# Optimization experiments

Measured on AMD Instinct MI355X. Metric: run time of the kernel, lower is better.

The kernel has to match this reference:

```python
import jax, jax.numpy as jnp
import numpy as np

B_BASE = 512   # queries
F_IN = 16      # incoming beam width
F_OUT = 16     # outgoing beam width (cfg.B)
D = 128        # vector dim
DH = 256       # MLP hidden dim
KCB = 4096     # codebook size
A = 32         # n_codes: approximate top-k shortlist
M = 2          # previous code steps
L = 2          # residual blocks


def setup_inputs() -> dict:
    key = jax.random.key(0)
    ks = jax.random.split(key, 16)
    s = 0.05
    return {
        "x_BD": jax.random.normal(ks[0], (B_BASE, D), jnp.float32),
        "xhat_BFD": jax.random.normal(ks[1], (B_BASE, F_IN, D), jnp.float32),
        "codes_MBF": jax.random.randint(ks[2], (M, B_BASE, F_IN), 0, KCB),
        "codebook": jax.random.normal(ks[3], (KCB, D), jnp.float32) * s,
        "codebook_rq": jax.random.normal(ks[4], (KCB, D), jnp.float32) * s,
        "in_w": jax.random.normal(ks[5], (D, DH), jnp.float32) * s,
        "in_b": jnp.zeros((DH,), jnp.float32),
        "cc_w": jax.random.normal(ks[6], (DH + D, DH), jnp.float32) * s,
        "cc_b": jnp.zeros((DH,), jnp.float32),
        "rb_w1": jax.random.normal(ks[7], (L, DH, DH), jnp.float32) * s,
        "rb_b1": jnp.zeros((L, DH), jnp.float32),
        "rb_w2": jax.random.normal(ks[8], (L, DH, DH), jnp.float32) * s,
        "rb_b2": jnp.zeros((L, DH), jnp.float32),
        "out_w": jax.random.normal(ks[9], (DH, D), jnp.float32) * s,
        "out_b": jnp.zeros((D,), jnp.float32),
    }


def reference(x_BD, xhat_BFD, codes_MBF, codebook, codebook_rq,
              in_w, in_b, cc_w, cc_b, rb_w1, rb_b1, rb_w2, rb_b2,
              out_w, out_b):
    B_base, F, Dd = xhat_BFD.shape
    B = B_base * F
    xhat_BD = xhat_BFD.reshape(B, Dd)

    # --- stage 1: approximate pairwise distance (drops ||x||^2 term) + shortlist topk ---
    xt_BD = (x_BD[:, None, :] - xhat_BFD).reshape(B, Dd)           # residual targets
    cb_sq = jnp.sum(codebook_rq * codebook_rq, axis=-1)             # [K]
    dists_BK = cb_sq[None, :] - 2.0 * (xt_BD @ codebook_rq.T)       # [B, K]
    _, top_codes_BA = jax.lax.top_k(-dists_BK, A)                   # smallest-A -> [B, A]

    # --- stage 2: gather codewords, run small residual MLP on candidates ---
    cw_in = codebook[top_codes_BA].reshape(B_base, F, A, Dd)        # [Bb,F,A,D]
    h = cw_in @ in_w + in_b                                         # in_proj -> [Bb,F,A,DH]
    xb = jnp.broadcast_to(xhat_BFD[:, :, None, :], (B_base, F, A, Dd))
    h = jnp.concatenate([h, xb], axis=-1) @ cc_w + cc_b             # concat block
    for i in range(rb_w1.shape[0]):
        h = h + jax.nn.relu(h @ rb_w1[i] + rb_b1[i]) @ rb_w2[i] + rb_b2[i]
    cw = h @ out_w + out_b + cw_in                                   # out_proj + residual codeword

    # --- stage 3: exact-ish distance over beam*A candidates + beam topk ---
    cw = cw.reshape(B, A, Dd) + xhat_BD[:, None, :]                  # candidate reconstructions
    cw_flat = cw.reshape(B_base, F * A, Dd)
    d2 = jnp.sum(cw_flat * cw_flat, axis=-1) - 2.0 * jnp.einsum('bd,bkd->bk', x_BD, cw_flat)
    _, idx_BF = jax.lax.top_k(-d2, F_OUT)                            # [Bb, F_OUT]

    # --- stage 4: regather codes and reconstructions for surviving beams ---
    codes_g_BF = jnp.take_along_axis(top_codes_BA.reshape(B_base, F * A), idx_BF, axis=-1)
    codes_rep = jnp.repeat(codes_MBF, A, axis=-1)                    # [M,Bb,F*A]
    idx_M = jnp.broadcast_to(idx_BF[None], (codes_MBF.shape[0], B_base, F_OUT))
    codes_sel = jnp.take_along_axis(codes_rep, idx_M, axis=-1)       # [M,Bb,F_OUT]
    xhat_next = jnp.take_along_axis(cw_flat, idx_BF[:, :, None], axis=1)  # [Bb,F_OUT,D]
    codes_out = jnp.concatenate([codes_sel, codes_g_BF[None]], axis=0)    # [M+1,Bb,F_OUT]
    return xhat_next, codes_out
```

## Files before the change

### kernel.cpp

```cpp
#include <hip/hip_runtime.h>
#include <float.h>

typedef unsigned int u32;
typedef unsigned long long u64;
typedef unsigned short u16;
typedef __attribute__((ext_vector_type(8))) short s16x8;
typedef __attribute__((ext_vector_type(4))) float f32x4;


static __device__ __forceinline__ u32 ordu(float f) {
  u32 u = __float_as_uint(f);
  return u ^ (u32)(((int)u >> 31) | (int)0x80000000);
}
static __device__ __forceinline__ u16 f2bf(float f) {
  u32 b = __float_as_uint(f);
  b += 0x7fffu + ((b >> 16) & 1u);
  return (u16)(b >> 16);
}


__global__ __launch_bounds__(256) void k_cbrqT(const float* __restrict__ cbrq,
                                               float* __restrict__ cbT,
                                               float* __restrict__ cb_sq) {
  __shared__ float tile[128 * 33];
  const int k0 = blockIdx.x * 32;
  const int t = threadIdx.x;
#pragma unroll
  for (int rep = 0; rep < 16; ++rep) {
    const int flat = rep * 256 + t;
    const int kk = flat >> 7, d = flat & 127;
    tile[d * 33 + kk] = cbrq[(k0 + kk) * 128 + d];
  }
  __syncthreads();
#pragma unroll
  for (int rep = 0; rep < 16; ++rep) {
    const int flat = rep * 256 + t;
    const int d = flat >> 5, kk = flat & 31;
    cbT[d * 4096 + k0 + kk] = tile[d * 33 + kk];
  }
  if (t < 32) {
    float r[8];
#pragma unroll
    for (int j = 0; j < 8; ++j) {
      const float v = tile[j * 33 + t];
      r[j] = __fmul_rn(v, v);
    }
    for (int i = 8; i < 128; i += 8) {
#pragma unroll
      for (int j = 0; j < 8; ++j) {
        const float v = tile[(i + j) * 33 + t];
        r[j] = __fadd_rn(r[j], __fmul_rn(v, v));
      }
    }
    cb_sq[k0 + t] = __fadd_rn(
        __fadd_rn(__fadd_rn(r[0], r[1]), __fadd_rn(r[2], r[3])),
        __fadd_rn(__fadd_rn(r[4], r[5]), __fadd_rn(r[6], r[7])));
  }
}

__global__ __launch_bounds__(256) void k_codeh(const float* __restrict__ cb,
                                               const float* __restrict__ in_w,
                                               const float* __restrict__ in_b,
                                               const float* __restrict__ cc_w,
                                               float* __restrict__ tmp_h,
                                               float* __restrict__ P) {
  __shared__ float row[128];
  __shared__ float th[256];
  const int code = blockIdx.x;
  const int t = threadIdx.x;
  if (t < 128) row[t] = cb[code * 128 + t];
  __syncthreads();
  float a = 0.f;
  for (int d = 0; d < 128; ++d) a = __builtin_fmaf(row[d], in_w[d * 256 + t], a);
  const float thv = __fadd_rn(a, in_b[t]);
  tmp_h[code * 256 + t] = thv;
  th[t] = thv;
  __syncthreads();
  float p = 0.f;
  for (int i = 0; i < 256; i += 4) {
    const float w0 = cc_w[(i + 0) * 256 + t], w1 = cc_w[(i + 1) * 256 + t];
    const float w2 = cc_w[(i + 2) * 256 + t], w3 = cc_w[(i + 3) * 256 + t];
    p = __builtin_fmaf(th[i + 0], w0, p);
    p = __builtin_fmaf(th[i + 1], w1, p);
    p = __builtin_fmaf(th[i + 2], w2, p);
    p = __builtin_fmaf(th[i + 3], w3, p);
  }
  P[code * 256 + t] = p;
}

__global__ __launch_bounds__(256) void k_pack(const float* __restrict__ rb_w1,
                                              const float* __restrict__ out_w,
                                              float* __restrict__ Wcat) {
  const int i = blockIdx.x;
  const int t = threadIdx.x;
  Wcat[i * 640 + t] = rb_w1[i * 256 + t];
  Wcat[i * 640 + 256 + t] = rb_w1[65536 + i * 256 + t];
  if (t < 128) Wcat[i * 640 + 512 + t] = out_w[i * 128 + t];
}

__global__ __launch_bounds__(256) void k_biasprep(
    const float* __restrict__ rb_b1, const float* __restrict__ rb_b2,
    const float* __restrict__ rb_w1, const float* __restrict__ out_w,
    const float* __restrict__ out_b, const float* __restrict__ cc_b,
    const float* __restrict__ Wcat, float* __restrict__ cvec) {
  const int t = threadIdx.x;
  const float* w11 = rb_w1 + 65536;
  float b2v = rb_b1[256 + t];
  for (int i = 0; i < 256; ++i) b2v += rb_b2[i] * w11[i * 256 + t];
  float c0 = rb_b1[t], c1 = b2v;
  for (int i = 0; i < 256; ++i) {
    const float cbi = cc_b[i];
    c0 += cbi * Wcat[i * 640 + t];
    c1 += cbi * Wcat[i * 640 + 256 + t];
  }
  cvec[t] = c0;
  cvec[256 + t] = c1;
  if (t < 128) {
    float bDv = out_b[t];
    for (int i = 0; i < 256; ++i)
      bDv += (rb_b2[i] + rb_b2[256 + i]) * out_w[i * 128 + t];
    float c2 = bDv;
    for (int i = 0; i < 256; ++i) c2 += cc_b[i] * Wcat[i * 640 + 512 + t];
    cvec[512 + t] = c2;
  }
}

__global__ __launch_bounds__(256) void k_wfrag(
    const float* __restrict__ W21, const float* __restrict__ V1,
    const float* __restrict__ V2, u16* __restrict__ W21f,
    u16* __restrict__ V1f, u16* __restrict__ V2f) {
  const int gid = blockIdx.x * 256 + threadIdx.x;
  const int l = gid & 63;
  const int grp = gid >> 6;
  const int kq = (l >> 4) * 8;
  const int nn = l & 15;
  if (grp < 128) {
    const int kt = grp >> 4, nt = grp & 15;
    u16* dst = W21f + (size_t)(grp * 64 + l) * 8;
#pragma unroll
    for (int j = 0; j < 8; ++j)
      dst[j] = f2bf(W21[(kt * 32 + kq + j) * 256 + nt * 16 + nn]);
  } else if (grp < 192) {
    const int g2 = grp - 128, kt = g2 >> 3, nt = g2 & 7;
    u16* dst = V1f + (size_t)(g2 * 64 + l) * 8;
#pragma unroll
    for (int j = 0; j < 8; ++j)
      dst[j] = f2bf(V1[(kt * 32 + kq + j) * 128 + nt * 16 + nn]);
  } else {
    const int g2 = grp - 192, kt = g2 >> 3, nt = g2 & 7;
    u16* dst = V2f + (size_t)(g2 * 64 + l) * 8;
#pragma unroll
    for (int j = 0; j < 8; ++j)
      dst[j] = f2bf(V2[(kt * 32 + kq + j) * 128 + nt * 16 + nn]);
  }
}

__global__ __launch_bounds__(256, 4) void gemm_f32(
    const float* __restrict__ Am, const float* __restrict__ Bm,
    float* __restrict__ Cm, const int Mi, const int Ni, const int Ki,
    const float* __restrict__ bias, const float* __restrict__ addm) {
  __shared__ float As[16][68];
  __shared__ float Bs[16][68];
  const int m0 = blockIdx.x * 64, n0 = blockIdx.y * 64;
  const int t = threadIdx.x;
  const int tm = (t & 15) * 4, tn = (t >> 4) * 4;
  float acc[4][4] = {};
  for (int k0 = 0; k0 < Ki; k0 += 16) {
    {
      const int row = t >> 2, q = t & 3;
      const float4 a4 = *(const float4*)(Am + (size_t)(m0 + row) * Ki + k0 + q * 4);
      As[q * 4 + 0][row] = a4.x; As[q * 4 + 1][row] = a4.y;
      As[q * 4 + 2][row] = a4.z; As[q * 4 + 3][row] = a4.w;
      const int kk = t >> 4, n4 = t & 15;
      *(float4*)&Bs[kk][n4 * 4] =
          *(const float4*)(Bm + (size_t)(k0 + kk) * Ni + n0 + n4 * 4);
    }
    __syncthreads();
#pragma unroll
    for (int kk = 0; kk < 16; ++kk) {
      const float4 av = *(const float4*)&As[kk][tm];
      const float4 bv = *(const float4*)&Bs[kk][tn];
      const float aa[4] = {av.x, av.y, av.z, av.w};
      const float bb[4] = {bv.x, bv.y, bv.z, bv.w};
#pragma unroll
      for (int i = 0; i < 4; ++i)
#pragma unroll
        for (int j = 0; j < 4; ++j) acc[i][j] += aa[i] * bb[j];
    }
    __syncthreads();
  }
#pragma unroll
  for (int i = 0; i < 4; ++i) {
    const int m = m0 + tm + i;
#pragma unroll
    for (int j = 0; j < 4; ++j) {
      const int n = n0 + tn + j;
      float v = acc[i][j];
      if (bias) v += bias[n];
      if (addm) v += addm[(size_t)m * Ni + n];
      Cm[(size_t)m * Ni + n] = v;
    }
  }
}

__global__ __launch_bounds__(256, 4) void gemm_scatter(
    const float* __restrict__ Am, const float* __restrict__ Bm, const int Mi,
    const int Ki, const float* __restrict__ bias,
    const float* __restrict__ add3, float* __restrict__ O1,
    float* __restrict__ O2, float* __restrict__ O3) {
  __shared__ float As[16][68];
  __shared__ float Bs[16][68];
  const int m0 = blockIdx.x * 64, n0 = blockIdx.y * 64;
  const int t = threadIdx.x;
  const int tm = (t & 15) * 4, tn = (t >> 4) * 4;
  float acc[4][4] = {};
  for (int k0 = 0; k0 < Ki; k0 += 16) {
    {
      const int row = t >> 2, q = t & 3;
      const float4 a4 = *(const float4*)(Am + (size_t)(m0 + row) * Ki + k0 + q * 4);
      As[q * 4 + 0][row] = a4.x; As[q * 4 + 1][row] = a4.y;
      As[q * 4 + 2][row] = a4.z; As[q * 4 + 3][row] = a4.w;
      const int kk = t >> 4, n4 = t & 15;
      *(float4*)&Bs[kk][n4 * 4] =
          *(const float4*)(Bm + (size_t)(k0 + kk) * 640 + n0 + n4 * 4);
    }
    __syncthreads();
#pragma unroll
    for (int kk = 0; kk < 16; ++kk) {
      const float4 av = *(const float4*)&As[kk][tm];
      const float4 bv = *(const float4*)&Bs[kk][tn];
      const float aa[4] = {av.x, av.y, av.z, av.w};
      const float bb[4] = {bv.x, bv.y, bv.z, bv.w};
#pragma unroll
      for (int i = 0; i < 4; ++i)
#pragma unroll
        for (int j = 0; j < 4; ++j) acc[i][j] += aa[i] * bb[j];
    }
    __syncthreads();
  }
#pragma unroll
  for (int i = 0; i < 4; ++i) {
    const int m = m0 + tm + i;
#pragma unroll
    for (int j = 0; j < 4; ++j) {
      const int n = n0 + tn + j;
      float v = acc[i][j];
      if (bias) v += bias[n];
      if (n < 256) {
        O1[(size_t)m * 256 + n] = v;
      } else if (n < 512) {
        O2[(size_t)m * 256 + n - 256] = v;
      } else {
        if (add3) v += add3[(size_t)m * 128 + n - 512];
        O3[(size_t)m * 128 + n - 512] = v;
      }
    }
  }
}

__global__ __launch_bounds__(512, 2) void k_stage1(
    const float* __restrict__ x, const float* __restrict__ xhat,
    const float* __restrict__ cbT, const float* __restrict__ cb_sq,
    int* __restrict__ topc) {
  __shared__ u32 distL[4 * 4096];
  __shared__ float xtL[512];
  const int r0 = blockIdx.x * 4;
  const int t = threadIdx.x;
  {
    const int rr = r0 + (t >> 7), d = t & 127;
    xtL[t] = __fsub_rn(x[(rr >> 4) * 128 + d], xhat[rr * 128 + d]);
  }
  __syncthreads();
  {
    const int k0 = t * 8;
    float acc[4][8] = {};
    for (int d = 0; d < 128; ++d) {
      const float4 c0 = *(const float4*)&cbT[d * 4096 + k0];
      const float4 c1 = *(const float4*)&cbT[d * 4096 + k0 + 4];
      const float cv[8] = {c0.x, c0.y, c0.z, c0.w, c1.x, c1.y, c1.z, c1.w};
      const float x0 = xtL[d], x1 = xtL[128 + d], x2 = xtL[256 + d],
                  x3 = xtL[384 + d];
#pragma unroll
      for (int j = 0; j < 8; ++j) {
        acc[0][j] = __builtin_fmaf(x0, cv[j], acc[0][j]);
        acc[1][j] = __builtin_fmaf(x1, cv[j], acc[1][j]);
        acc[2][j] = __builtin_fmaf(x2, cv[j], acc[2][j]);
        acc[3][j] = __builtin_fmaf(x3, cv[j], acc[3][j]);
      }
    }
    const float4 s0 = *(const float4*)&cb_sq[k0];
    const float4 s1 = *(const float4*)&cb_sq[k0 + 4];
    const float cs[8] = {s0.x, s0.y, s0.z, s0.w, s1.x, s1.y, s1.z, s1.w};
#pragma unroll
    for (int rr = 0; rr < 4; ++rr)
#pragma unroll
      for (int j = 0; j < 8; ++j)
        distL[rr * 4096 + k0 + j] =
            ordu(__fsub_rn(cs[j], __fmul_rn(2.0f, acc[rr][j])));
  }
  __syncthreads();
  const int w = t >> 6, lane = t & 63;
  if (w < 4) {
    u32* dr = distL + w * 4096;
    u64 m1 = ~0ull, m2 = ~0ull;
    for (int e = 0; e < 64; ++e) {
      const int idx = e * 64 + lane;
      const u64 key = ((u64)dr[idx] << 32) | (u32)idx;
      if (key < m1) { m2 = m1; m1 = key; } else if (key < m2) { m2 = key; }
    }
    bool have2 = true;
    for (int it = 0; it < 32; ++it) {
      u64 g = m1;
#pragma unroll
      for (int sh = 1; sh < 64; sh <<= 1) {
        const u64 o = __shfl_xor(g, sh);
        g = (o < g) ? o : g;
      }
      const int bi = (int)(g & 0xFFFFFFFFu);
      if (lane == 0) topc[(r0 + w) * 32 + it] = bi;
      if ((bi & 63) == lane) {
        dr[bi] = 0xFFFFFFFFu;
        if (have2) {
          m1 = m2; m2 = ~0ull; have2 = false;
        } else {
          m1 = m2 = ~0ull;
          for (int e = 0; e < 64; ++e) {
            const int idx = e * 64 + lane;
            const u64 key = ((u64)dr[idx] << 32) | (u32)idx;
            if (key < m1) { m2 = m1; m1 = key; } else if (key < m2) { m2 = key; }
          }
          have2 = true;
        }
      }
    }
  }
}

__global__ __launch_bounds__(256, 4) void k_mlp(
    const int* __restrict__ topc, const float* __restrict__ A1,
    const float* __restrict__ A2, const float* __restrict__ B1,
    const float* __restrict__ B2, const float* __restrict__ Dc,
    const float* __restrict__ Dr, const u16* __restrict__ W21f,
    const u16* __restrict__ V1f, const u16* __restrict__ V2f,
    const float* __restrict__ xhat, const float* __restrict__ x,
    float* __restrict__ d2g) {
  __shared__ __align__(16) u16 abuf[32 * 264];
  __shared__ float B1r[256];
  __shared__ int codesL[32];
  __shared__ float d2red[32][4];

  const int tt = threadIdx.x;
  const int br = blockIdx.x;
  const int bb = br >> 4;
  const int w = tt >> 6, l = tt & 63;

  B1r[tt] = B1[br * 256 + tt];
  if (tt < 32) codesL[tt] = topc[br * 32 + tt];
  __syncthreads();

  {
    const int c = tt & 31, g = tt >> 5;
    const int code = codesL[c];
    const float4* A14 = (const float4*)(A1 + code * 256 + g * 32);
    u32* dst = (u32*)(abuf + c * 264 + g * 32);
#pragma unroll
// ... 37 lines not shown

  f32x4 acc2f[2][2];
#pragma unroll
  for (int mt = 0; mt < 2; ++mt)
#pragma unroll
    for (int ntl = 0; ntl < 2; ++ntl) acc2f[mt][ntl] = zero4;
  for (int kt = 0; kt < 8; ++kt) {
    const s16x8 a0 = *(const s16x8*)(abuf + arow * 264 + kt * 32 + kq);
    const s16x8 a1 = *(const s16x8*)(abuf + (16 + arow) * 264 + kt * 32 + kq);
#pragma unroll
    for (int ntl = 0; ntl < 2; ++ntl) {
      const s16x8 b = v1f[(kt * 8 + w * 2 + ntl) * 64 + l];
      acc2f[0][ntl] = __builtin_amdgcn_mfma_f32_16x16x32_bf16(
          a0, b, acc2f[0][ntl], 0, 0, 0);
      acc2f[1][ntl] = __builtin_amdgcn_mfma_f32_16x16x32_bf16(
          a1, b, acc2f[1][ntl], 0, 0, 0);
    }
  }

  u16 r2v[2][4][4];
#pragma unroll
  for (int mt = 0; mt < 2; ++mt)
#pragma unroll
    for (int ntl = 0; ntl < 4; ++ntl) {
      const int n = w * 64 + ntl * 16 + arow;
      const float b2 = B2[br * 256 + n];
      const f32x4 cf = accf[mt][ntl];
#pragma unroll
      for (int rg = 0; rg < 4; ++rg) {
        const int m = mt * 16 + (l >> 4) * 4 + rg;
        const float a2 = A2[codesL[m] * 256 + n];
        r2v[mt][ntl][rg] = f2bf(fmaxf(cf[rg] + a2 + b2, 0.f));
      }
    }
  __syncthreads();
#pragma unroll
  for (int mt = 0; mt < 2; ++mt)
#pragma unroll
    for (int ntl = 0; ntl < 4; ++ntl) {
      const int n = w * 64 + ntl * 16 + arow;
#pragma unroll
      for (int rg = 0; rg < 4; ++rg) {
        const int m = mt * 16 + (l >> 4) * 4 + rg;
        abuf[m * 264 + n] = r2v[mt][ntl][rg];
      }
    }
  __syncthreads();

  for (int kt = 0; kt < 8; ++kt) {
    const s16x8 a0 = *(const s16x8*)(abuf + arow * 264 + kt * 32 + kq);
    const s16x8 a1 = *(const s16x8*)(abuf + (16 + arow) * 264 + kt * 32 + kq);
#pragma unroll
    for (int ntl = 0; ntl < 2; ++ntl) {
      const s16x8 b = v2f[(kt * 8 + w * 2 + ntl) * 64 + l];
      acc2f[0][ntl] = __builtin_amdgcn_mfma_f32_16x16x32_bf16(
          a0, b, acc2f[0][ntl], 0, 0, 0);
      acc2f[1][ntl] = __builtin_amdgcn_mfma_f32_16x16x32_bf16(
          a1, b, acc2f[1][ntl], 0, 0, 0);
    }
  }

  float sm[2][4];
#pragma unroll
  for (int mt = 0; mt < 2; ++mt)
#pragma unroll
    for (int rg = 0; rg < 4; ++rg) sm[mt][rg] = 0.f;
#pragma unroll
  for (int ntl = 0; ntl < 2; ++ntl) {
    const int d = w * 32 + ntl * 16 + arow;
    const float dr = Dr[br * 128 + d];
    const float xh = xhat[br * 128 + d];
    const float xq = x[bb * 128 + d];
#pragma unroll
    for (int mt = 0; mt < 2; ++mt) {
      const f32x4 cf = acc2f[mt][ntl];
#pragma unroll
      for (int rg = 0; rg < 4; ++rg) {
        const int m = mt * 16 + (l >> 4) * 4 + rg;
        const float cand = cf[rg] + Dc[codesL[m] * 128 + d] + dr + xh;
        sm[mt][rg] += cand * cand - 2.f * xq * cand;
      }
    }
  }
#pragma unroll
  for (int mt = 0; mt < 2; ++mt)
#pragma unroll
    for (int rg = 0; rg < 4; ++rg) {
      float s = sm[mt][rg];
      s += __shfl_xor(s, 1);
      s += __shfl_xor(s, 2);
      s += __shfl_xor(s, 4);
      s += __shfl_xor(s, 8);
      if (arow == 0) d2red[mt * 16 + (l >> 4) * 4 + rg][w] = s;
    }
  __syncthreads();
  if (tt < 32)
    d2g[bb * 512 + (br & 15) * 32 + tt] =
        d2red[tt][0] + d2red[tt][1] + d2red[tt][2] + d2red[tt][3];
}

__global__ __launch_bounds__(64, 1) void k_sel32(const float* __restrict__ d2g,
                                                 int* __restrict__ sel32) {
  __shared__ u32 d2u[512];
  const int bb = blockIdx.x;
  const int t = threadIdx.x;
  for (int i = t; i < 512; i += 64) d2u[i] = ordu(d2g[bb * 512 + i]);
  __syncthreads();
  for (int it = 0; it < 32; ++it) {
    u64 m = ~0ull;
#pragma unroll
    for (int e = 0; e < 8; ++e) {
      const int idx = e * 64 + t;
      const u64 key = ((u64)d2u[idx] << 32) | (u32)idx;
      m = (key < m) ? key : m;
    }
#pragma unroll
    for (int sh = 1; sh < 64; sh <<= 1) {
      const u64 o = __shfl_xor(m, sh);
      m = (o < m) ? o : m;
    }
    const int s = (int)(m & 0xFFFFFFFFu);
    if ((s & 63) == t) d2u[s] = 0xFFFFFFFFu;
    if (t == 0) sel32[bb * 32 + it] = s;
  }
}

__global__ __launch_bounds__(256, 5) void k_rescore(
    const int* __restrict__ sel32, const int* __restrict__ topc,
    const float* __restrict__ P, const float* __restrict__ cb,
    const float* __restrict__ xhat, const float* __restrict__ x,
    const float* __restrict__ cc_w, const float* __restrict__ cc_b,
    const float* __restrict__ rb_w1, const float* __restrict__ rb_b1,
    const float* __restrict__ rb_w2, const float* __restrict__ rb_b2,
    const float* __restrict__ out_w, const float* __restrict__ out_b,
    float* __restrict__ d2r, float* __restrict__ candv) {
  __shared__ float A_[8][256], B_[8][256], C_[8][256];
  __shared__ float xhL[8][128], xqL[128];
  __shared__ int codeL[8], rowL[8];
  const int bb = blockIdx.x >> 2;
  const int j0 = (blockIdx.x & 3) * 8;
  const int t = threadIdx.x;
  if (t < 8) {
    const int s = sel32[bb * 32 + j0 + t];
    rowL[t] = bb * 16 + (s >> 5);
    codeL[t] = topc[(bb * 16 + (s >> 5)) * 32 + (s & 31)];
  }
  if (t < 128) xqL[t] = x[bb * 128 + t];
  __syncthreads();
  for (int idx = t; idx < 1024; idx += 256) {
    const int c = idx >> 7, d = idx & 127;
    xhL[c][d] = xhat[rowL[c] * 128 + d];
  }
  __syncthreads();
  {
    float acc[8];
#pragma unroll
    for (int c = 0; c < 8; ++c) acc[c] = P[codeL[c] * 256 + t];
    for (int d = 0; d < 128; d += 4) {
      const float w0 = cc_w[(256 + d + 0) * 256 + t];
      const float w1 = cc_w[(256 + d + 1) * 256 + t];
      const float w2 = cc_w[(256 + d + 2) * 256 + t];
      const float w3 = cc_w[(256 + d + 3) * 256 + t];
#pragma unroll
      for (int c = 0; c < 8; ++c) {
        const float4 h = *(const float4*)&xhL[c][d];
        acc[c] = __builtin_fmaf(h.x, w0, acc[c]);
        acc[c] = __builtin_fmaf(h.y, w1, acc[c]);
        acc[c] = __builtin_fmaf(h.z, w2, acc[c]);
        acc[c] = __builtin_fmaf(h.w, w3, acc[c]);
      }
    }
    const float b = cc_b[t];
#pragma unroll
    for (int c = 0; c < 8; ++c) B_[c][t] = __fadd_rn(acc[c], b);
  }
  __syncthreads();
  {
    float acc[8] = {};
    for (int i = 0; i < 256; i += 4) {
      const float w0 = rb_w1[(i + 0) * 256 + t], w1 = rb_w1[(i + 1) * 256 + t];
      const float w2 = rb_w1[(i + 2) * 256 + t], w3 = rb_w1[(i + 3) * 256 + t];
#pragma unroll
      for (int c = 0; c < 8; ++c) {
        const float4 h = *(const float4*)&B_[c][i];
        acc[c] = __builtin_fmaf(h.x, w0, acc[c]);
        acc[c] = __builtin_fmaf(h.y, w1, acc[c]);
        acc[c] = __builtin_fmaf(h.z, w2, acc[c]);
        acc[c] = __builtin_fmaf(h.w, w3, acc[c]);
      }
    }
    const float b = rb_b1[t];
#pragma unroll
    for (int c = 0; c < 8; ++c) C_[c][t] = fmaxf(__fadd_rn(acc[c], b), 0.f);
  }
  __syncthreads();
  {
    float acc[8] = {};
    for (int i = 0; i < 256; i += 4) {
      const float w0 = rb_w2[(i + 0) * 256 + t], w1 = rb_w2[(i + 1) * 256 + t];
      const float w2 = rb_w2[(i + 2) * 256 + t], w3 = rb_w2[(i + 3) * 256 + t];
#pragma unroll
      for (int c = 0; c < 8; ++c) {
        const float4 h = *(const float4*)&C_[c][i];
        acc[c] = __builtin_fmaf(h.x, w0, acc[c]);
        acc[c] = __builtin_fmaf(h.y, w1, acc[c]);
        acc[c] = __builtin_fmaf(h.z, w2, acc[c]);
        acc[c] = __builtin_fmaf(h.w, w3, acc[c]);
      }
    }
    const float b = rb_b2[t];
#pragma unroll
    for (int c = 0; c < 8; ++c)
      A_[c][t] = __fadd_rn(__fadd_rn(B_[c][t], acc[c]), b);
  }
  __syncthreads();
  {
    float acc[8] = {};
    const float* w11 = rb_w1 + 65536;
    for (int i = 0; i < 256; i += 4) {
      const float w0 = w11[(i + 0) * 256 + t], w1 = w11[(i + 1) * 256 + t];
      const float w2 = w11[(i + 2) * 256 + t], w3 = w11[(i + 3) * 256 + t];
#pragma unroll
      for (int c = 0; c < 8; ++c) {
        const float4 h = *(const float4*)&A_[c][i];
        acc[c] = __builtin_fmaf(h.x, w0, acc[c]);
        acc[c] = __builtin_fmaf(h.y, w1, acc[c]);
        acc[c] = __builtin_fmaf(h.z, w2, acc[c]);
        acc[c] = __builtin_fmaf(h.w, w3, acc[c]);
      }
    }
    const float b = rb_b1[256 + t];
#pragma unroll
    for (int c = 0; c < 8; ++c) B_[c][t] = fmaxf(__fadd_rn(acc[c], b), 0.f);
  }
  __syncthreads();
  {
    float acc[8] = {};
    const float* w21 = rb_w2 + 65536;
    for (int i = 0; i < 256; i += 4) {
      const float w0 = w21[(i + 0) * 256 + t], w1 = w21[(i + 1) * 256 + t];
      const float w2 = w21[(i + 2) * 256 + t], w3 = w21[(i + 3) * 256 + t];
#pragma unroll
      for (int c = 0; c < 8; ++c) {
        const float4 h = *(const float4*)&B_[c][i];
        acc[c] = __builtin_fmaf(h.x, w0, acc[c]);
        acc[c] = __builtin_fmaf(h.y, w1, acc[c]);
        acc[c] = __builtin_fmaf(h.z, w2, acc[c]);
        acc[c] = __builtin_fmaf(h.w, w3, acc[c]);
      }
    }
    const float b = rb_b2[256 + t];
#pragma unroll
    for (int c = 0; c < 8; ++c)
      C_[c][t] = __fadd_rn(__fadd_rn(A_[c][t], acc[c]), b);
  }
  __syncthreads();
  if (t < 128) {
    float acc[8] = {};
    for (int i = 0; i < 256; i += 4) {
      const float w0 = out_w[(i + 0) * 128 + t], w1 = out_w[(i + 1) * 128 + t];
      const float w2 = out_w[(i + 2) * 128 + t], w3 = out_w[(i + 3) * 128 + t];
#pragma unroll
      for (int c = 0; c < 8; ++c) {
        const float4 h = *(const float4*)&C_[c][i];
        acc[c] = __builtin_fmaf(h.x, w0, acc[c]);
        acc[c] = __builtin_fmaf(h.y, w1, acc[c]);
        acc[c] = __builtin_fmaf(h.z, w2, acc[c]);
        acc[c] = __builtin_fmaf(h.w, w3, acc[c]);
      }
    }
    const float ob = out_b[t];
#pragma unroll
    for (int c = 0; c < 8; ++c) {
      const float cbv = cb[codeL[c] * 128 + t];
      const float cw_ = __fadd_rn(__fadd_rn(acc[c], ob), cbv);
      const float cand = __fadd_rn(cw_, xhL[c][t]);
      B_[c][t] = cand;
      candv[(bb * 32 + j0 + c) * 128 + t] = cand;
    }
  }
  __syncthreads();
  if (t < 8) {
    float r[8];
#pragma unroll
    for (int j = 0; j < 8; ++j) {
      const float v = B_[t][j];
      r[j] = __fmul_rn(v, v);
    }
    for (int i = 8; i < 128; i += 8) {
#pragma unroll
      for (int j = 0; j < 8; ++j) {
        const float v = B_[t][i + j];
        r[j] = __fadd_rn(r[j], __fmul_rn(v, v));
      }
    }
    const float s1f = __fadd_rn(
        __fadd_rn(__fadd_rn(r[0], r[1]), __fadd_rn(r[2], r[3])),
        __fadd_rn(__fadd_rn(r[4], r[5]), __fadd_rn(r[6], r[7])));
    double s2 = 0.0;
    for (int d = 0; d < 128; ++d)
      s2 += (double)xqL[d] * (double)B_[t][d];
    const float s2f = (float)s2;
    d2r[bb * 32 + j0 + t] = __fsub_rn(s1f, __fmul_rn(2.0f, s2f));
  }
}

__global__ __launch_bounds__(64, 1) void k_final(
    const float* __restrict__ d2r, const int* __restrict__ sel32,
    const int* __restrict__ topc, const int* __restrict__ codes_in,
    const float* __restrict__ candv, float* __restrict__ out) {
  __shared__ u32 winLo[16];
  const int bb = blockIdx.x;
  const int t = threadIdx.x;
  u64 key = ~0ull;
  if (t < 32) {
    const u32 s = (u32)sel32[bb * 32 + t];
    key = ((u64)ordu(d2r[bb * 32 + t]) << 32) | (s << 5) | (u32)t;
  }
  for (int it = 0; it < 16; ++it) {
    u64 m = key;
#pragma unroll
    for (int sh = 1; sh < 64; sh <<= 1) {
      const u64 o = __shfl_xor(m, sh);
      m = (o < m) ? o : m;
    }
    if (key == m) key = ~0ull;
    if (t == 0) winLo[it] = (u32)(m & 0xFFFFFFFFu);
  }
  __syncthreads();
  if (t < 16) {
    const u32 lo = winLo[t];
    const int s = (int)((lo >> 5) & 511u);
    const int f = s >> 5;
    const int code = topc[(bb * 16 + f) * 32 + (s & 31)];
    float* oc = out + 512 * 16 * 128;
    oc[bb * 16 + t] = (float)codes_in[bb * 16 + f];
    oc[8192 + bb * 16 + t] = (float)codes_in[8192 + bb * 16 + f];
    oc[16384 + bb * 16 + t] = (float)code;
  }
  __syncthreads();
  for (int idx = t; idx < 2048; idx += 64) {
    const int w_ = idx >> 7, d = idx & 127;
    const int j = (int)(winLo[w_] & 31u);
    out[(bb * 16 + w_) * 128 + d] = candv[(bb * 32 + j) * 128 + d];
  }
}

extern "C" void kernel_launch(void* const* d_in, const int* in_sizes, int n_in,
                              void* d_out, int out_size, void* d_ws,
                              size_t ws_size, hipStream_t stream) {
  const float* x = (const float*)d_in[0];
  const float* xhat = (const float*)d_in[1];
  const int* codes = (const int*)d_in[2];
  const float* cb = (const float*)d_in[3];
  const float* cbrq = (const float*)d_in[4];
  const float* in_w = (const float*)d_in[5];
  const float* in_b = (const float*)d_in[6];
  const float* cc_w = (const float*)d_in[7];
  const float* cc_b = (const float*)d_in[8];
  const float* rb_w1 = (const float*)d_in[9];
  const float* rb_b1 = (const float*)d_in[10];
  const float* rb_w2 = (const float*)d_in[11];
  const float* rb_b2 = (const float*)d_in[12];
  const float* out_w = (const float*)d_in[13];
  const float* out_b = (const float*)d_in[14];
  float* out = (float*)d_out;

  float* ws = (float*)d_ws;
  size_t o = 0;
  float* cb_sq = ws + o; o += 4096;
  float* P = ws + o;     o += (size_t)4096 * 256;
  float* cbT = ws + o;   const size_t cbT_off = o; o += (size_t)128 * 4096;
  float* tmp_h = ws + o; o += (size_t)4096 * 256;
  float* Wcat = ws + o;  o += (size_t)256 * 640;
  float* M_A = ws + o;   o += (size_t)256 * 640;
  float* M_B = ws + o;   o += (size_t)128 * 640;
  float* cvec = ws + o;  o += 640;
  float* A1 = ws + o;    o += (size_t)4096 * 256;
  float* A2 = ws + o;    o += (size_t)4096 * 256;
  float* Dc = ws + o;    o += (size_t)4096 * 128;
  float* B1 = ws + o;    o += (size_t)8192 * 256;
  float* B2 = ws + o;    o += (size_t)8192 * 256;
  float* Dr = ws + o;    o += (size_t)8192 * 128;
  float* W21 = ws + o;   o += 65536;
  float* V1 = ws + o;    o += 32768;
  float* V2 = ws + o;    o += 32768;
  int* topc = (int*)(ws + o); o += 262144;
  float* d2g = ws + o;   o += 262144;
  u16* W21f = (u16*)(ws + o); o += 32768;
  u16* V1f = (u16*)(ws + o);  o += 16384;
  u16* V2f = (u16*)(ws + o);  o += 16384;
  float* candv = ws + o; o += (size_t)16384 * 128;
  float* d2r = ws + cbT_off;
  int* sel32 = (int*)(ws + cbT_off + 16384);

  k_cbrqT<<<dim3(128), dim3(256), 0, stream>>>(cbrq, cbT, cb_sq);
  k_codeh<<<dim3(4096), dim3(256), 0, stream>>>(cb, in_w, in_b, cc_w, tmp_h, P);
  k_pack<<<dim3(256), dim3(256), 0, stream>>>(rb_w1, out_w, Wcat);
  k_biasprep<<<dim3(1), dim3(256), 0, stream>>>(rb_b1, rb_b2, rb_w1, out_w,
                                                out_b, cc_b, Wcat, cvec);
  gemm_f32<<<dim3(4, 10), dim3(256), 0, stream>>>(cc_w, Wcat, M_A, 256, 640,
                                                  256, nullptr, nullptr);
  gemm_f32<<<dim3(2, 10), dim3(256), 0, stream>>>(cc_w + 256 * 256, Wcat, M_B,
                                                  128, 640, 256, nullptr,
                                                  nullptr);
  gemm_scatter<<<dim3(64, 10), dim3(256), 0, stream>>>(
      tmp_h, M_A, 4096, 256, nullptr, cb, A1, A2, Dc);
  gemm_scatter<<<dim3(128, 10), dim3(256), 0, stream>>>(
      xhat, M_B, 8192, 128, cvec, nullptr, B1, B2, Dr);
  gemm_f32<<<dim3(4, 4), dim3(256), 0, stream>>>(rb_w2, rb_w1 + 65536, W21, 256,
                                                 256, 256, nullptr, nullptr);
  gemm_f32<<<dim3(4, 2), dim3(256), 0, stream>>>(rb_w2, out_w, V1, 256, 128,
                                                 256, nullptr, nullptr);
  gemm_f32<<<dim3(4, 2), dim3(256), 0, stream>>>(rb_w2 + 65536, out_w, V2, 256,
                                                 128, 256, nullptr, nullptr);
  k_wfrag<<<dim3(64), dim3(256), 0, stream>>>(W21, V1, V2, W21f, V1f, V2f);

  k_stage1<<<dim3(2048), dim3(512), 0, stream>>>(x, xhat, cbT, cb_sq, topc);
  k_mlp<<<dim3(8192), dim3(256), 0, stream>>>(topc, A1, A2, B1, B2, Dc, Dr,
                                              W21f, V1f, V2f, xhat, x, d2g);
  k_sel32<<<dim3(512), dim3(64), 0, stream>>>(d2g, sel32);
  k_rescore<<<dim3(2048), dim3(256), 0, stream>>>(
      sel32, topc, P, cb, xhat, x, cc_w, cc_b, rb_w1, rb_b1, rb_w2, rb_b2,
      out_w, out_b, d2r, candv);
  k_final<<<dim3(512), dim3(64), 0, stream>>>(d2r, sel32, topc, codes, candv,
                                              out);
  (void)in_sizes; (void)n_in; (void)out_size; (void)ws_size;
}
```

Baseline: 878.4 us.

## Merge prep kernels into one launch and restructure rescore MLP thread mapping

Folds the codebook transpose, code hidden projection, bias prep, weight packing and the W21/V1/V2 weight-product-plus-bf16-fragment kernels into a single multi-role k_prep1 launch. The bias prep now reads rb_w1 and out_w directly instead of depending on Wcat, which the fused kernel writes in parallel. The two scatter GEMMs are merged into one launch. The rescore MLP is remapped so each thread computes two output columns for four candidates instead of one column for eight, which changes register use and weight reuse. The aim is to cut launch count and serialization among small prep kernels, at the risk of slow naive per-thread fp32 weight products in the fused prep blocks.

```diff
diff --git a/kernel.cpp b/kernel.cpp
--- a/kernel.cpp
+++ b/kernel.cpp
@@ -18,140 +18,177 @@
   return (u16)(b >> 16);
 }
 
-
-__global__ __launch_bounds__(256) void k_cbrqT(const float* __restrict__ cbrq,
-                                               float* __restrict__ cbT,
-                                               float* __restrict__ cb_sq) {
-  __shared__ float tile[128 * 33];
-  const int k0 = blockIdx.x * 32;
+static __device__ __forceinline__ void layer_fma(
+    const float* __restrict__ src, int srcStride, int c0, int jc,
+    const float* __restrict__ wbase, int klen, float a0[4], float a1[4]) {
+  for (int i = 0; i < klen; i += 4) {
+    const float wa0 = wbase[(i + 0) * 256 + jc];
+    const float wa1 = wbase[(i + 1) * 256 + jc];
+    const float wa2 = wbase[(i + 2) * 256 + jc];
+    const float wa3 = wbase[(i + 3) * 256 + jc];
+    const float wb0 = wbase[(i + 0) * 256 + jc + 128];
+    const float wb1 = wbase[(i + 1) * 256 + jc + 128];
+    const float wb2 = wbase[(i + 2) * 256 + jc + 128];
+    const float wb3 = wbase[(i + 3) * 256 + jc + 128];
+#pragma unroll
+    for (int c4 = 0; c4 < 4; ++c4) {
+      const float4 h = *(const float4*)&src[(c0 + c4) * srcStride + i];
+      a0[c4] = __builtin_fmaf(h.x, wa0, a0[c4]);
+      a0[c4] = __builtin_fmaf(h.y, wa1, a0[c4]);
+      a0[c4] = __builtin_fmaf(h.z, wa2, a0[c4]);
+      a0[c4] = __builtin_fmaf(h.w, wa3, a0[c4]);
+      a1[c4] = __builtin_fmaf(h.x, wb0, a1[c4]);
+      a1[c4] = __builtin_fmaf(h.y, wb1, a1[c4]);
+      a1[c4] = __builtin_fmaf(h.z, wb2, a1[c4]);
+      a1[c4] = __builtin_fmaf(h.w, wb3, a1[c4]);
+    }
+  }
+}
+
+__global__ __launch_bounds__(256) void k_prep1(
+    const float* __restrict__ cbrq, float* __restrict__ cbT,
+    float* __restrict__ cb_sq, const float* __restrict__ cb,
+    const float* __restrict__ in_w, const float* __restrict__ in_b,
+    const float* __restrict__ cc_w, float* __restrict__ tmp_h,
+    float* __restrict__ P, const float* __restrict__ rb_b1,
+    const float* __restrict__ rb_b2, const float* __restrict__ rb_w1,
+    const float* __restrict__ out_w, const float* __restrict__ out_b,
+    const float* __restrict__ cc_b, float* __restrict__ cvec,
+    float* __restrict__ Wcat, const float* __restrict__ rb_w2,
+    u16* __restrict__ W21f, u16* __restrict__ V1f, u16* __restrict__ V2f) {
+  __shared__ float sh[128 * 33];
+  const int b = blockIdx.x;
   const int t = threadIdx.x;
-#pragma unroll
-  for (int rep = 0; rep < 16; ++rep) {
-    const int flat = rep * 256 + t;
-    const int kk = flat >> 7, d = flat & 127;
-    tile[d * 33 + kk] = cbrq[(k0 + kk) * 128 + d];
-  }
-  __syncthreads();
-#pragma unroll
-  for (int rep = 0; rep < 16; ++rep) {
-    const int flat = rep * 256 + t;
-    const int d = flat >> 5, kk = flat & 31;
-    cbT[d * 4096 + k0 + kk] = tile[d * 33 + kk];
-  }
-  if (t < 32) {
-    float r[8];
-#pragma unroll
-    for (int j = 0; j < 8; ++j) {
-      const float v = tile[j * 33 + t];
-      r[j] = __fmul_rn(v, v);
-    }
-    for (int i = 8; i < 128; i += 8) {
+  if (b < 128) {
+    const int k0 = b * 32;
+#pragma unroll
+    for (int rep = 0; rep < 16; ++rep) {
+      const int flat = rep * 256 + t;
+      const int kk = flat >> 7, d = flat & 127;
+      sh[d * 33 + kk] = cbrq[(k0 + kk) * 128 + d];
+    }
+    __syncthreads();
+#pragma unroll
+    for (int rep = 0; rep < 16; ++rep) {
+      const int flat = rep * 256 + t;
+      const int d = flat >> 5, kk = flat & 31;
+      cbT[d * 4096 + k0 + kk] = sh[d * 33 + kk];
+    }
+    if (t < 32) {
+      float r[8];
 #pragma unroll
       for (int j = 0; j < 8; ++j) {
-        const float v = tile[(i + j) * 33 + t];
-        r[j] = __fadd_rn(r[j], __fmul_rn(v, v));
-      }
-    }
-    cb_sq[k0 + t] = __fadd_rn(
-        __fadd_rn(__fadd_rn(r[0], r[1]), __fadd_rn(r[2], r[3])),
-        __fadd_rn(__fadd_rn(r[4], r[5]), __fadd_rn(r[6], r[7])));
-  }
-}
-
-__global__ __launch_bounds__(256) void k_codeh(const float* __restrict__ cb,
-                                               const float* __restrict__ in_w,
-                                               const float* __restrict__ in_b,
-                                               const float* __restrict__ cc_w,
-                                               float* __restrict__ tmp_h,
-                                               float* __restrict__ P) {
-  __shared__ float row[128];
-  __shared__ float th[256];
-  const int code = blockIdx.x;
-  const int t = threadIdx.x;
-  if (t < 128) row[t] = cb[code * 128 + t];
-  __syncthreads();
-  float a = 0.f;
-  for (int d = 0; d < 128; ++d) a = __builtin_fmaf(row[d], in_w[d * 256 + t], a);
-  const float thv = __fadd_rn(a, in_b[t]);
-  tmp_h[code * 256 + t] = thv;
-  th[t] = thv;
-  __syncthreads();
-  float p = 0.f;
-  for (int i = 0; i < 256; i += 4) {
-    const float w0 = cc_w[(i + 0) * 256 + t], w1 = cc_w[(i + 1) * 256 + t];
-    const float w2 = cc_w[(i + 2) * 256 + t], w3 = cc_w[(i + 3) * 256 + t];
-    p = __builtin_fmaf(th[i + 0], w0, p);
-    p = __builtin_fmaf(th[i + 1], w1, p);
-    p = __builtin_fmaf(th[i + 2], w2, p);
-    p = __builtin_fmaf(th[i + 3], w3, p);
-  }
-  P[code * 256 + t] = p;
-}
-
-__global__ __launch_bounds__(256) void k_pack(const float* __restrict__ rb_w1,
-                                              const float* __restrict__ out_w,
-                                              float* __restrict__ Wcat) {
-  const int i = blockIdx.x;
-  const int t = threadIdx.x;
-  Wcat[i * 640 + t] = rb_w1[i * 256 + t];
-  Wcat[i * 640 + 256 + t] = rb_w1[65536 + i * 256 + t];
-  if (t < 128) Wcat[i * 640 + 512 + t] = out_w[i * 128 + t];
-}
-
-__global__ __launch_bounds__(256) void k_biasprep(
-    const float* __restrict__ rb_b1, const float* __restrict__ rb_b2,
-    const float* __restrict__ rb_w1, const float* __restrict__ out_w,
-    const float* __restrict__ out_b, const float* __restrict__ cc_b,
-    const float* __restrict__ Wcat, float* __restrict__ cvec) {
-  const int t = threadIdx.x;
-  const float* w11 = rb_w1 + 65536;
-  float b2v = rb_b1[256 + t];
-  for (int i = 0; i < 256; ++i) b2v += rb_b2[i] * w11[i * 256 + t];
-  float c0 = rb_b1[t], c1 = b2v;
-  for (int i = 0; i < 256; ++i) {
-    const float cbi = cc_b[i];
-    c0 += cbi * Wcat[i * 640 + t];
-    c1 += cbi * Wcat[i * 640 + 256 + t];
-  }
-  cvec[t] = c0;
-  cvec[256 + t] = c1;
-  if (t < 128) {
-    float bDv = out_b[t];
-    for (int i = 0; i < 256; ++i)
-      bDv += (rb_b2[i] + rb_b2[256 + i]) * out_w[i * 128 + t];
-    float c2 = bDv;
-    for (int i = 0; i < 256; ++i) c2 += cc_b[i] * Wcat[i * 640 + 512 + t];
-    cvec[512 + t] = c2;
-  }
-}
-
-__global__ __launch_bounds__(256) void k_wfrag(
-    const float* __restrict__ W21, const float* __restrict__ V1,
-    const float* __restrict__ V2, u16* __restrict__ W21f,
-    u16* __restrict__ V1f, u16* __restrict__ V2f) {
-  const int gid = blockIdx.x * 256 + threadIdx.x;
-  const int l = gid & 63;
-  const int grp = gid >> 6;
-  const int kq = (l >> 4) * 8;
-  const int nn = l & 15;
-  if (grp < 128) {
-    const int kt = grp >> 4, nt = grp & 15;
-    u16* dst = W21f + (size_t)(grp * 64 + l) * 8;
-#pragma unroll
-    for (int j = 0; j < 8; ++j)
-      dst[j] = f2bf(W21[(kt * 32 + kq + j) * 256 + nt * 16 + nn]);
-  } else if (grp < 192) {
-    const int g2 = grp - 128, kt = g2 >> 3, nt = g2 & 7;
-    u16* dst = V1f + (size_t)(g2 * 64 + l) * 8;
-#pragma unroll
-    for (int j = 0; j < 8; ++j)
-      dst[j] = f2bf(V1[(kt * 32 + kq + j) * 128 + nt * 16 + nn]);
+        const float v = sh[j * 33 + t];
+        r[j] = __fmul_rn(v, v);
+      }
+      for (int i = 8; i < 128; i += 8) {
+#pragma unroll
+        for (int j = 0; j < 8; ++j) {
+          const float v = sh[(i + j) * 33 + t];
+          r[j] = __fadd_rn(r[j], __fmul_rn(v, v));
+        }
+      }
+      cb_sq[k0 + t] = __fadd_rn(
+          __fadd_rn(__fadd_rn(r[0], r[1]), __fadd_rn(r[2], r[3])),
+          __fadd_rn(__fadd_rn(r[4], r[5]), __fadd_rn(r[6], r[7])));
+    }
+  } else if (b < 4224) {
+    const int code = b - 128;
+    float* row = sh;
+    float* th = sh + 128;
+    if (t < 128) row[t] = cb[code * 128 + t];
+    __syncthreads();
+    float a = 0.f;
+    for (int d = 0; d < 128; ++d)
+      a = __builtin_fmaf(row[d], in_w[d * 256 + t], a);
+    const float thv = __fadd_rn(a, in_b[t]);
+    tmp_h[code * 256 + t] = thv;
+    th[t] = thv;
+    __syncthreads();
+    float p = 0.f;
+    for (int i = 0; i < 256; i += 4) {
+      const float w0 = cc_w[(i + 0) * 256 + t], w1 = cc_w[(i + 1) * 256 + t];
+      const float w2 = cc_w[(i + 2) * 256 + t], w3 = cc_w[(i + 3) * 256 + t];
+      p = __builtin_fmaf(th[i + 0], w0, p);
+      p = __builtin_fmaf(th[i + 1], w1, p);
+      p = __builtin_fmaf(th[i + 2], w2, p);
+      p = __builtin_fmaf(th[i + 3], w3, p);
+    }
+    P[code * 256 + t] = p;
+  } else if (b == 4224) {
+    const float* w11 = rb_w1 + 65536;
+    float b2v = rb_b1[256 + t];
+    for (int i = 0; i < 256; ++i) b2v += rb_b2[i] * w11[i * 256 + t];
+    float c0 = rb_b1[t], c1 = b2v;
+    for (int i = 0; i < 256; ++i) {
+      const float cbi = cc_b[i];
+      c0 += cbi * rb_w1[i * 256 + t];
+      c1 += cbi * w11[i * 256 + t];
+    }
+    cvec[t] = c0;
+    cvec[256 + t] = c1;
+    if (t < 128) {
+      float bDv = out_b[t];
+      for (int i = 0; i < 256; ++i)
+        bDv += (rb_b2[i] + rb_b2[256 + i]) * out_w[i * 128 + t];
+      float c2 = bDv;
+      for (int i = 0; i < 256; ++i) c2 += cc_b[i] * out_w[i * 128 + t];
+      cvec[512 + t] = c2;
+    }
+  } else if (b < 4481) {
+    const int i = b - 4225;
+    Wcat[i * 640 + t] = rb_w1[i * 256 + t];
+    Wcat[i * 640 + 256 + t] = rb_w1[65536 + i * 256 + t];
+    if (t < 128) Wcat[i * 640 + 512 + t] = out_w[i * 128 + t];
   } else {
-    const int g2 = grp - 192, kt = g2 >> 3, nt = g2 & 7;
-    u16* dst = V2f + (size_t)(g2 * 64 + l) * 8;
-#pragma unroll
-    for (int j = 0; j < 8; ++j)
-      dst[j] = f2bf(V2[(kt * 32 + kq + j) * 128 + nt * 16 + nn]);
+    const int gid = (b - 4481) * 256 + t;
+    const int l = gid & 63;
+    const int grp = gid >> 6;
+    const int kq = (l >> 4) * 8;
+    const int nn = l & 15;
+    float acc[8] = {};
+    if (grp < 128) {
+      const int kt = grp >> 4, nt = grp & 15;
+      const int col = nt * 16 + nn;
+      const int r0 = kt * 32 + kq;
+      const float* w11 = rb_w1 + 65536;
+      for (int k = 0; k < 256; ++k) {
+        const float wv = w11[k * 256 + col];
+#pragma unroll
+        for (int j = 0; j < 8; ++j)
+          acc[j] = __builtin_fmaf(rb_w2[(r0 + j) * 256 + k], wv, acc[j]);
+      }
+      u16* dst = W21f + (size_t)(grp * 64 + l) * 8;
+#pragma unroll
+      for (int j = 0; j < 8; ++j) dst[j] = f2bf(acc[j]);
+    } else if (grp < 192) {
+      const int g2 = grp - 128, kt = g2 >> 3, nt = g2 & 7;
+      const int col = nt * 16 + nn;
+      const int r0 = kt * 32 + kq;
+      for (int k = 0; k < 256; ++k) {
+        const float wv = out_w[k * 128 + col];
+#pragma unroll
+        for (int j = 0; j < 8; ++j)
+          acc[j] = __builtin_fmaf(rb_w2[(r0 + j) * 256 + k], wv, acc[j]);
+      }
+      u16* dst = V1f + (size_t)(g2 * 64 + l) * 8;
+#pragma unroll
+      for (int j = 0; j < 8; ++j) dst[j] = f2bf(acc[j]);
+    } else {
+      const int g2 = grp - 192, kt = g2 >> 3, nt = g2 & 7;
+      const int col = nt * 16 + nn;
+      const int r0 = kt * 32 + kq;
+      const float* w21 = rb_w2 + 65536;
+      for (int k = 0; k < 256; ++k) {
+        const float wv = out_w[k * 128 + col];
+#pragma unroll
+        for (int j = 0; j < 8; ++j)
+          acc[j] = __builtin_fmaf(w21[(r0 + j) * 256 + k], wv, acc[j]);
+      }
+      u16* dst = V2f + (size_t)(g2 * 64 + l) * 8;
+#pragma unroll
+      for (int j = 0; j < 8; ++j) dst[j] = f2bf(acc[j]);
+    }
   }
 }
 
@@ -203,14 +240,25 @@
   }
 }
 
-__global__ __launch_bounds__(256, 4) void gemm_scatter(
-    const float* __restrict__ Am, const float* __restrict__ Bm, const int Mi,
-    const int Ki, const float* __restrict__ bias,
-    const float* __restrict__ add3, float* __restrict__ O1,
-    float* __restrict__ O2, float* __restrict__ O3) {
+__global__ __launch_bounds__(256, 4) void gemm_scatter2(
+    const float* __restrict__ tmp_h, const float* __restrict__ M_A,
+    const float* __restrict__ xhat, const float* __restrict__ M_B,
+    const float* __restrict__ cvec, const float* __restrict__ cb,
+    float* __restrict__ A1, float* __restrict__ A2, float* __restrict__ Dc,
+    float* __restrict__ B1, float* __restrict__ B2, float* __restrict__ Dr) {
   __shared__ float As[16][68];
   __shared__ float Bs[16][68];
-  const int m0 = blockIdx.x * 64, n0 = blockIdx.y * 64;
+  const bool isA = blockIdx.x < 64;
+  const float* Am = isA ? tmp_h : xhat;
+  const float* Bm = isA ? M_A : M_B;
+  const int Ki = isA ? 256 : 128;
+  const float* bias = isA ? nullptr : cvec;
+  const float* add3 = isA ? cb : nullptr;
+  float* O1 = isA ? A1 : B1;
+  float* O2 = isA ? A2 : B2;
+  float* O3 = isA ? Dc : Dr;
+  const int m0 = (isA ? blockIdx.x : blockIdx.x - 64) * 64;
+  const int n0 = blockIdx.y * 64;
   const int t = threadIdx.x;
   const int tm = (t & 15) * 4, tn = (t >> 4) * 4;
   float acc[4][4] = {};
@@ -554,131 +602,100 @@
     xhL[c][d] = xhat[rowL[c] * 128 + d];
   }
   __syncthreads();
+  const int hc = t >> 7;
+  const int c0 = hc * 4;
+  const int jc = t & 127;
+  float a0[4], a1[4];
+
+#pragma unroll
+  for (int c4 = 0; c4 < 4; ++c4) {
+    a0[c4] = P[codeL[c0 + c4] * 256 + jc];
+    a1[c4] = P[codeL[c0 + c4] * 256 + jc + 128];
+  }
+  layer_fma(&xhL[0][0], 128, c0, jc, cc_w + 256 * 256, 128, a0, a1);
   {
-    float acc[8];
-#pragma unroll
-    for (int c = 0; c < 8; ++c) acc[c] = P[codeL[c] * 256 + t];
-    for (int d = 0; d < 128; d += 4) {
-      const float w0 = cc_w[(256 + d + 0) * 256 + t];
-      const float w1 = cc_w[(256 + d + 1) * 256 + t];
-      const float w2 = cc_w[(256 + d + 2) * 256 + t];
-      const float w3 = cc_w[(256 + d + 3) * 256 + t];
-#pragma unroll
-      for (int c = 0; c < 8; ++c) {
-        const float4 h = *(const float4*)&xhL[c][d];
-        acc[c] = __builtin_fmaf(h.x, w0, acc[c]);
-        acc[c] = __builtin_fmaf(h.y, w1, acc[c]);
-        acc[c] = __builtin_fmaf(h.z, w2, acc[c]);
-        acc[c] = __builtin_fmaf(h.w, w3, acc[c]);
-      }
-    }
-    const float b = cc_b[t];
-#pragma unroll
-    for (int c = 0; c < 8; ++c) B_[c][t] = __fadd_rn(acc[c], b);
-  }
-  __syncthreads();
+    const float ba = cc_b[jc], bbv = cc_b[jc + 128];
+#pragma unroll
+    for (int c4 = 0; c4 < 4; ++c4) {
+      B_[c0 + c4][jc] = __fadd_rn(a0[c4], ba);
+      B_[c0 + c4][jc + 128] = __fadd_rn(a1[c4], bbv);
+    }
+  }
+  __syncthreads();
+#pragma unroll
+  for (int c4 = 0; c4 < 4; ++c4) { a0[c4] = 0.f; a1[c4] = 0.f; }
+  layer_fma(&B_[0][0], 256, c0, jc, rb_w1, 256, a0, a1);
   {
-    float acc[8] = {};
+    const float ba = rb_b1[jc], bbv = rb_b1[jc + 128];
+#pragma unroll
+    for (int c4 = 0; c4 < 4; ++c4) {
+      C_[c0 + c4][jc] = fmaxf(__fadd_rn(a0[c4], ba), 0.f);
+      C_[c0 + c4][jc + 128] = fmaxf(__fadd_rn(a1[c4], bbv), 0.f);
+    }
+  }
+  __syncthreads();
+#pragma unroll
+  for (int c4 = 0; c4 < 4; ++c4) { a0[c4] = 0.f; a1[c4] = 0.f; }
+  layer_fma(&C_[0][0], 256, c0, jc, rb_w2, 256, a0, a1);
+  {
+    const float ba = rb_b2[jc], bbv = rb_b2[jc + 128];
+#pragma unroll
+    for (int c4 = 0; c4 < 4; ++c4) {
+      A_[c0 + c4][jc] = __fadd_rn(__fadd_rn(B_[c0 + c4][jc], a0[c4]), ba);
+      A_[c0 + c4][jc + 128] =
+          __fadd_rn(__fadd_rn(B_[c0 + c4][jc + 128], a1[c4]), bbv);
+    }
+  }
+  __syncthreads();
+#pragma unroll
+  for (int c4 = 0; c4 < 4; ++c4) { a0[c4] = 0.f; a1[c4] = 0.f; }
+  layer_fma(&A_[0][0], 256, c0, jc, rb_w1 + 65536, 256, a0, a1);
+  {
+    const float ba = rb_b1[256 + jc], bbv = rb_b1[256 + jc + 128];
+#pragma unroll
+    for (int c4 = 0; c4 < 4; ++c4) {
+      B_[c0 + c4][jc] = fmaxf(__fadd_rn(a0[c4], ba), 0.f);
+      B_[c0 + c4][jc + 128] = fmaxf(__fadd_rn(a1[c4], bbv), 0.f);
+    }
+  }
+  __syncthreads();
+#pragma unroll
+  for (int c4 = 0; c4 < 4; ++c4) { a0[c4] = 0.f; a1[c4] = 0.f; }
+  layer_fma(&B_[0][0], 256, c0, jc, rb_w2 + 65536, 256, a0, a1);
+  {
+    const float ba = rb_b2[256 + jc], bbv = rb_b2[256 + jc + 128];
+#pragma unroll
+    for (int c4 = 0; c4 < 4; ++c4) {
+      C_[c0 + c4][jc] = __fadd_rn(__fadd_rn(A_[c0 + c4][jc], a0[c4]), ba);
+      C_[c0 + c4][jc + 128] =
+          __fadd_rn(__fadd_rn(A_[c0 + c4][jc + 128], a1[c4]), bbv);
+    }
+  }
+  __syncthreads();
+  {
+    const int d = jc;
+    float acc[4] = {};
     for (int i = 0; i < 256; i += 4) {
-      const float w0 = rb_w1[(i + 0) * 256 + t], w1 = rb_w1[(i + 1) * 256 + t];
-      const float w2 = rb_w1[(i + 2) * 256 + t], w3 = rb_w1[(i + 3) * 256 + t];
-#pragma unroll
-      for (int c = 0; c < 8; ++c) {
-        const float4 h = *(const float4*)&B_[c][i];
-        acc[c] = __builtin_fmaf(h.x, w0, acc[c]);
-        acc[c] = __builtin_fmaf(h.y, w1, acc[c]);
-        acc[c] = __builtin_fmaf(h.z, w2, acc[c]);
-        acc[c] = __builtin_fmaf(h.w, w3, acc[c]);
-      }
-    }
-    const float b = rb_b1[t];
-#pragma unroll
-    for (int c = 0; c < 8; ++c) C_[c][t] = fmaxf(__fadd_rn(acc[c], b), 0.f);
-  }
-  __syncthreads();
-  {
-    float acc[8] = {};
-    for (int i = 0; i < 256; i += 4) {
-      const float w0 = rb_w2[(i + 0) * 256 + t], w1 = rb_w2[(i + 1) * 256 + t];
-      const float w2 = rb_w2[(i + 2) * 256 + t], w3 = rb_w2[(i + 3) * 256 + t];
-#pragma unroll
-      for (int c = 0; c < 8; ++c) {
-        const float4 h = *(const float4*)&C_[c][i];
-        acc[c] = __builtin_fmaf(h.x, w0, acc[c]);
-        acc[c] = __builtin_fmaf(h.y, w1, acc[c]);
-        acc[c] = __builtin_fmaf(h.z, w2, acc[c]);
-        acc[c] = __builtin_fmaf(h.w, w3, acc[c]);
-      }
-    }
-    const float b = rb_b2[t];
-#pragma unroll
-    for (int c = 0; c < 8; ++c)
-      A_[c][t] = __fadd_rn(__fadd_rn(B_[c][t], acc[c]), b);
-  }
-  __syncthreads();
-  {
-    float acc[8] = {};
-    const float* w11 = rb_w1 + 65536;
-    for (int i = 0; i < 256; i += 4) {
-      const float w0 = w11[(i + 0) * 256 + t], w1 = w11[(i + 1) * 256 + t];
-      const float w2 = w11[(i + 2) * 256 + t], w3 = w11[(i + 3) * 256 + t];
-#pragma unroll
-      for (int c = 0; c < 8; ++c) {
-        const float4 h = *(const float4*)&A_[c][i];
-        acc[c] = __builtin_fmaf(h.x, w0, acc[c]);
-        acc[c] = __builtin_fmaf(h.y, w1, acc[c]);
-        acc[c] = __builtin_fmaf(h.z, w2, acc[c]);
-        acc[c] = __builtin_fmaf(h.w, w3, acc[c]);
-      }
-    }
-    const float b = rb_b1[256 + t];
-#pragma unroll
-    for (int c = 0; c < 8; ++c) B_[c][t] = fmaxf(__fadd_rn(acc[c], b), 0.f);
-  }
-  __syncthreads();
-  {
-    float acc[8] = {};
-    const float* w21 = rb_w2 + 65536;
-    for (int i = 0; i < 256; i += 4) {
-      const float w0 = w21[(i + 0) * 256 + t], w1 = w21[(i + 1) * 256 + t];
-      const float w2 = w21[(i + 2) * 256 + t], w3 = w21[(i + 3) * 256 + t];
-#pragma unroll
-      for (int c = 0; c < 8; ++c) {
-        const float4 h = *(const float4*)&B_[c][i];
-        acc[c] = __builtin_fmaf(h.x, w0, acc[c]);
-        acc[c] = __builtin_fmaf(h.y, w1, acc[c]);
-        acc[c] = __builtin_fmaf(h.z, w2, acc[c]);
-        acc[c] = __builtin_fmaf(h.w, w3, acc[c]);
-      }
-    }
-    const float b = rb_b2[256 + t];
-#pragma unroll
-    for (int c = 0; c < 8; ++c)
-      C_[c][t] = __fadd_rn(__fadd_rn(A_[c][t], acc[c]), b);
-  }
-  __syncthreads();
-  if (t < 128) {
-    float acc[8] = {};
-    for (int i = 0; i < 256; i += 4) {
-      const float w0 = out_w[(i + 0) * 128 + t], w1 = out_w[(i + 1) * 128 + t];
-      const float w2 = out_w[(i + 2) * 128 + t], w3 = out_w[(i + 3) * 128 + t];
-#pragma unroll
-      for (int c = 0; c < 8; ++c) {
-        const float4 h = *(const float4*)&C_[c][i];
-        acc[c] = __builtin_fmaf(h.x, w0, acc[c]);
-        acc[c] = __builtin_fmaf(h.y, w1, acc[c]);
-        acc[c] = __builtin_fmaf(h.z, w2, acc[c]);
-        acc[c] = __builtin_fmaf(h.w, w3, acc[c]);
-      }
-    }
-    const float ob = out_b[t];
-#pragma unroll
-    for (int c = 0; c < 8; ++c) {
-      const float cbv = cb[codeL[c] * 128 + t];
-      const float cw_ = __fadd_rn(__fadd_rn(acc[c], ob), cbv);
-      const float cand = __fadd_rn(cw_, xhL[c][t]);
-      B_[c][t] = cand;
-      candv[(bb * 32 + j0 + c) * 128 + t] = cand;
+      const float w0 = out_w[(i + 0) * 128 + d], w1 = out_w[(i + 1) * 128 + d];
+      const float w2 = out_w[(i + 2) * 128 + d], w3 = out_w[(i + 3) * 128 + d];
+#pragma unroll
+      for (int c4 = 0; c4 < 4; ++c4) {
+        const float4 h = *(const float4*)&C_[c0 + c4][i];
+        acc[c4] = __builtin_fmaf(h.x, w0, acc[c4]);
+        acc[c4] = __builtin_fmaf(h.y, w1, acc[c4]);
+        acc[c4] = __builtin_fmaf(h.z, w2, acc[c4]);
+        acc[c4] = __builtin_fmaf(h.w, w3, acc[c4]);
+      }
+    }
+    const float ob = out_b[d];
+#pragma unroll
+    for (int c4 = 0; c4 < 4; ++c4) {
+      const int c = c0 + c4;
+      const float cbv = cb[codeL[c] * 128 + d];
+      const float cw_ = __fadd_rn(__fadd_rn(acc[c4], ob), cbv);
+      const float cand = __fadd_rn(cw_, xhL[c][d]);
+      B_[c][d] = cand;
+      candv[(bb * 32 + j0 + c) * 128 + d] = cand;
     }
   }
   __syncthreads();
@@ -784,9 +801,6 @@
   float* B1 = ws + o;    o += (size_t)8192 * 256;
   float* B2 = ws + o;    o += (size_t)8192 * 256;
   float* Dr = ws + o;    o += (size_t)8192 * 128;
-  float* W21 = ws + o;   o += 65536;
-  float* V1 = ws + o;    o += 32768;
-  float* V2 = ws + o;    o += 32768;
   int* topc = (int*)(ws + o); o += 262144;
   float* d2g = ws + o;   o += 262144;
   u16* W21f = (u16*)(ws + o); o += 32768;
@@ -796,27 +810,16 @@
   float* d2r = ws + cbT_off;
   int* sel32 = (int*)(ws + cbT_off + 16384);
 
-  k_cbrqT<<<dim3(128), dim3(256), 0, stream>>>(cbrq, cbT, cb_sq);
-  k_codeh<<<dim3(4096), dim3(256), 0, stream>>>(cb, in_w, in_b, cc_w, tmp_h, P);
-  k_pack<<<dim3(256), dim3(256), 0, stream>>>(rb_w1, out_w, Wcat);
-  k_biasprep<<<dim3(1), dim3(256), 0, stream>>>(rb_b1, rb_b2, rb_w1, out_w,
-                                                out_b, cc_b, Wcat, cvec);
+  k_prep1<<<dim3(4545), dim3(256), 0, stream>>>(
+      cbrq, cbT, cb_sq, cb, in_w, in_b, cc_w, tmp_h, P, rb_b1, rb_b2, rb_w1,
+      out_w, out_b, cc_b, cvec, Wcat, rb_w2, W21f, V1f, V2f);
   gemm_f32<<<dim3(4, 10), dim3(256), 0, stream>>>(cc_w, Wcat, M_A, 256, 640,
                                                   256, nullptr, nullptr);
   gemm_f32<<<dim3(2, 10), dim3(256), 0, stream>>>(cc_w + 256 * 256, Wcat, M_B,
                                                   128, 640, 256, nullptr,
                                                   nullptr);
-  gemm_scatter<<<dim3(64, 10), dim3(256), 0, stream>>>(
-      tmp_h, M_A, 4096, 256, nullptr, cb, A1, A2, Dc);
-  gemm_scatter<<<dim3(128, 10), dim3(256), 0, stream>>>(
-      xhat, M_B, 8192, 128, cvec, nullptr, B1, B2, Dr);
-  gemm_f32<<<dim3(4, 4), dim3(256), 0, stream>>>(rb_w2, rb_w1 + 65536, W21, 256,
-                                                 256, 256, nullptr, nullptr);
-  gemm_f32<<<dim3(4, 2), dim3(256), 0, stream>>>(rb_w2, out_w, V1, 256, 128,
-                                                 256, nullptr, nullptr);
-  gemm_f32<<<dim3(4, 2), dim3(256), 0, stream>>>(rb_w2 + 65536, out_w, V2, 256,
-                                                 128, 256, nullptr, nullptr);
-  k_wfrag<<<dim3(64), dim3(256), 0, stream>>>(W21, V1, V2, W21f, V1f, V2f);
+  gemm_scatter2<<<dim3(192, 10), dim3(256), 0, stream>>>(
+      tmp_h, M_A, xhat, M_B, cvec, cb, A1, A2, Dc, B1, B2, Dr);
 
   k_stage1<<<dim3(2048), dim3(512), 0, stream>>>(x, xhat, cbT, cb_sq, topc);
   k_mlp<<<dim3(8192), dim3(256), 0, stream>>>(topc, A1, A2, B1, B2, Dc, Dr,
```

Result: faster. 773.5 us (median of 3 runs) (-11.9%).
